# Performance work log

Hardware: AMD Instinct MI355X
Metric: run time of the kernel (lower is better)

The kernel has to match this reference:

```python
import jax, jax.numpy as jnp
import numpy as np

EMBED_DIM = 1024
NUM_HEADS = 16
D_K = EMBED_DIM // NUM_HEADS
FFN_DIM = 4096
EPS = 1e-5


def _linear_params(key, fan_in, fan_out):
    kw, kb = jax.random.split(key)
    bound = 1.0 / np.sqrt(fan_in)
    W = jax.random.uniform(kw, (fan_out, fan_in), jnp.float32, -bound, bound)
    b = jax.random.uniform(kb, (fan_out,), jnp.float32, -bound, bound)
    return W, b


def setup_inputs() -> dict:
    key = jax.random.key(0)
    ks = jax.random.split(key, 8)
    x = jax.random.normal(ks[0], (2, 2048, EMBED_DIM), jnp.float32)
    Wq, bq = _linear_params(ks[1], EMBED_DIM, EMBED_DIM)
    Wk, bk = _linear_params(ks[2], EMBED_DIM, EMBED_DIM)
    Wv, bv = _linear_params(ks[3], EMBED_DIM, EMBED_DIM)
    Wo, bo = _linear_params(ks[4], EMBED_DIM, EMBED_DIM)
    W1, b1 = _linear_params(ks[5], EMBED_DIM, FFN_DIM)
    W2, b2 = _linear_params(ks[6], FFN_DIM, EMBED_DIM)
    g1 = jnp.ones((EMBED_DIM,), jnp.float32)
    be1 = jnp.zeros((EMBED_DIM,), jnp.float32)
    g2 = jnp.ones((EMBED_DIM,), jnp.float32)
    be2 = jnp.zeros((EMBED_DIM,), jnp.float32)
    return {"x": x, "Wq": Wq, "bq": bq, "Wk": Wk, "bk": bk, "Wv": Wv, "bv": bv,
            "Wo": Wo, "bo": bo, "W1": W1, "b1": b1, "W2": W2, "b2": b2,
            "g1": g1, "be1": be1, "g2": g2, "be2": be2}


def _layernorm(x, g, b):
    mu = jnp.mean(x, axis=-1, keepdims=True)
    var = jnp.var(x, axis=-1, keepdims=True)
    return (x - mu) * jax.lax.rsqrt(var + EPS) * g + b


def reference(x, Wq, bq, Wk, bk, Wv, bv, Wo, bo, W1, b1, W2, b2, g1, be1, g2, be2):
    B, S, _ = x.shape
    h = _layernorm(x, g1, be1)
    # qkv projections -> [B, H, S, d_k]
    def split_heads(t):
        return t.reshape(B, S, NUM_HEADS, D_K).transpose(0, 2, 1, 3)
    q = split_heads(h @ Wq.T + bq)
    k = split_heads(h @ Wk.T + bk)
    v = split_heads(h @ Wv.T + bv)
    scores = jnp.einsum('bhqd,bhkd->bhqk', q, k) / np.sqrt(D_K).astype(np.float32)
    attn = jax.nn.softmax(scores, axis=-1)
    out = jnp.einsum('bhqk,bhkd->bhqd', attn, v)
    out = out.transpose(0, 2, 1, 3).reshape(B, S, EMBED_DIM)
    attn_out = out @ Wo.T + bo
    x = x + attn_out
    h2 = _layernorm(x, g2, be2)
    ffn = jax.nn.relu(h2 @ W1.T + b1) @ W2.T + b2
    return x + ffn
```

## Files before the change

kernel.cpp:

```cpp
#include <hip/hip_runtime.h>

typedef __attribute__((ext_vector_type(8))) short short8;
typedef __attribute__((ext_vector_type(4))) float f32x4;
typedef __attribute__((ext_vector_type(4))) unsigned short us4;

#define MFMA_BF16(a, b, c) __builtin_amdgcn_mfma_f32_16x16x32_bf16((a), (b), (c), 0, 0, 0)

__device__ __forceinline__ unsigned short f2bf(float f) {
  union { float f; unsigned int u; } x; x.f = f;
  unsigned int r = x.u + 0x7FFFu + ((x.u >> 16) & 1u);
  return (unsigned short)(r >> 16);
}
__device__ __forceinline__ float bf2f(unsigned short b) {
  union { float f; unsigned int u; } x; x.u = ((unsigned int)b) << 16;
  return x.f;
}

typedef __attribute__((address_space(3))) unsigned int lds_uint;
typedef const __attribute__((address_space(1))) unsigned int gbl_uint;

__device__ __forceinline__ void gload_lds16(const void* g, void* l) {
  __builtin_amdgcn_global_load_lds((gbl_uint*)g, (lds_uint*)l, 16, 0, 0);
}

__device__ __forceinline__ short8 lds_swz_read(const unsigned short* base, int row, int colbyte) {
  return *(const short8*)((const char*)base + row * 128 + (colbyte ^ ((row & 7) << 4)));
}

__global__ __launch_bounds__(256) void cvt_all(const float* __restrict__ Wq,
                                               const float* __restrict__ Wk,
                                               const float* __restrict__ Wv,
                                               const float* __restrict__ Wo,
                                               const float* __restrict__ W1,
                                               const float* __restrict__ W2,
                                               unsigned short* __restrict__ Wqkv_b,
                                               unsigned short* __restrict__ Wo_b,
                                               unsigned short* __restrict__ W1_b,
                                               unsigned short* __restrict__ W2_b) {
  const int b = blockIdx.x;
  const float* src;
  unsigned short* dst;
  int off;
  if (b < 1024)      { src = Wq; dst = Wqkv_b;           off = b; }
  else if (b < 2048) { src = Wk; dst = Wqkv_b + 1048576; off = b - 1024; }
  else if (b < 3072) { src = Wv; dst = Wqkv_b + 2097152; off = b - 2048; }
  else if (b < 4096) { src = Wo; dst = Wo_b;             off = b - 3072; }
  else if (b < 8192) { src = W1; dst = W1_b;             off = b - 4096; }
  else               { src = W2; dst = W2_b;             off = b - 8192; }
  const int i = off * 256 + threadIdx.x;
  const float4 v = ((const float4*)src)[i];
  us4 o;
  o.x = f2bf(v.x); o.y = f2bf(v.y); o.z = f2bf(v.z); o.w = f2bf(v.w);
  ((us4*)dst)[i] = o;
}

__global__ __launch_bounds__(256) void ln_kernel(const float* __restrict__ x,
                                                 const float* __restrict__ g,
                                                 const float* __restrict__ be,
                                                 unsigned short* __restrict__ out) {
  const int row = blockIdx.x;
  const int t = threadIdx.x;
  const float4 v = ((const float4*)(x + (size_t)row * 1024))[t];
  float s = v.x + v.y + v.z + v.w;
  float s2 = v.x * v.x + v.y * v.y + v.z * v.z + v.w * v.w;
#pragma unroll
  for (int d = 1; d < 64; d <<= 1) {
    s += __shfl_xor(s, d);
    s2 += __shfl_xor(s2, d);
  }
  __shared__ float red[8];
  const int wid = t >> 6, lane = t & 63;
  if (lane == 0) { red[wid] = s; red[4 + wid] = s2; }
  __syncthreads();
  s = red[0] + red[1] + red[2] + red[3];
  s2 = red[4] + red[5] + red[6] + red[7];
  const float mu = s * (1.0f / 1024.0f);
  const float var = s2 * (1.0f / 1024.0f) - mu * mu;
  const float rstd = rsqrtf(var + 1e-5f);
  const float4 gv = ((const float4*)g)[t];
  const float4 bv = ((const float4*)be)[t];
  us4 o;
  o.x = f2bf((v.x - mu) * rstd * gv.x + bv.x);
  o.y = f2bf((v.y - mu) * rstd * gv.y + bv.y);
  o.z = f2bf((v.z - mu) * rstd * gv.z + bv.z);
  o.w = f2bf((v.w - mu) * rstd * gv.w + bv.w);
  ((us4*)(out + (size_t)row * 1024))[t] = o;
}

__global__ __launch_bounds__(256) void ffn2_reduce(float* __restrict__ out,
                                                   const float* __restrict__ p1,
                                                   const float* __restrict__ x1,
                                                   const float* __restrict__ b2) {
  const int row = blockIdx.x, t = threadIdx.x;
  const size_t i = (size_t)row * 256 + t;
  float4 v = ((const float4*)out)[i];
  const float4 a = ((const float4*)p1)[i];
  const float4 c = ((const float4*)x1)[i];
  const float4 b = ((const float4*)b2)[t];
  v.x += a.x + c.x + b.x; v.y += a.y + c.y + b.y;
  v.z += a.z + c.z + b.z; v.w += a.w + c.w + b.w;
  ((float4*)out)[i] = v;
}

template <int BN, int EPI>
__global__ __launch_bounds__(256, 2) void gemm_bf16(const unsigned short* __restrict__ A,
                                                    const unsigned short* __restrict__ B,
                                                    const float* __restrict__ bias,
                                                    const float* __restrict__ biasK,
                                                    const float* __restrict__ biasV,
                                                    const float* __restrict__ res,
                                                    void* __restrict__ outp,
                                                    int M, int N, int K,
                                                    int gx, int gy, int kspl) {
  constexpr int WN = (BN == 128) ? 2 : 1;
  constexpr int WROWS = 128 / (4 / WN);
  constexpr int MW = WROWS / 16;
  constexpr int NW = (BN / WN) / 16;
  constexpr int BCH = BN / 32;
  constexpr int LOADS = 4 + BCH;

  __shared__ __align__(16) unsigned short As[2][128 * 64];
  __shared__ __align__(16) unsigned short Bs[2][BN * 64];

  const int nwg = gridDim.x;
  const int id2 = ((int)blockIdx.x & 7) * (nwg >> 3) + ((int)blockIdx.x >> 3);
  const int bx = id2 % gx;
  const int byz = id2 / gx;
  const int by = byz % gy;
  const int bz = byz / gy;

  const int wid = threadIdx.x >> 6;
  const int lane = threadIdx.x & 63;
  const int lr = lane & 15, lg = lane >> 4;
  const int row0 = by * 128;
  const int col0 = bx * BN;
  const int k0 = bz * kspl;
  const int wm = (wid / WN) * WROWS;
  const int wn = (wid % WN) * (BN / WN);

  const int scol = ((lane & 7) ^ ((lane >> 3) & 7)) * 8;

  auto stage = [&](int buf, int kt) {
#pragma unroll
    for (int i = 0; i < 4; ++i) {
      const int r = wid * 32 + i * 8;
      gload_lds16(A + (size_t)(row0 + r + (lane >> 3)) * K + kt + scol,
                  (void*)&As[buf][r * 64]);
    }
#pragma unroll
    for (int i = 0; i < BCH; ++i) {
      const int r = wid * (8 * BCH) + i * 8;
      gload_lds16(B + (size_t)(col0 + r + (lane >> 3)) * K + kt + scol,
                  (void*)&Bs[buf][r * 64]);
    }
  };

  f32x4 acc[MW][NW];
#pragma unroll
  for (int m = 0; m < MW; ++m)
#pragma unroll
    for (int n = 0; n < NW; ++n) acc[m][n] = (f32x4){0.f, 0.f, 0.f, 0.f};

  auto mma = [&](int buf) {
#pragma unroll
    for (int kk = 0; kk < 64; kk += 32) {
      const int colbyte = kk * 2 + lg * 16;
      short8 av[MW], bv[NW];
#pragma unroll
      for (int m = 0; m < MW; ++m)
        av[m] = lds_swz_read(&As[buf][0], wm + m * 16 + lr, colbyte);
#pragma unroll
      for (int n = 0; n < NW; ++n)
        bv[n] = lds_swz_read(&Bs[buf][0], wn + n * 16 + lr, colbyte);
#pragma unroll
      for (int m = 0; m < MW; ++m)
#pragma unroll
        for (int n = 0; n < NW; ++n) acc[m][n] = MFMA_BF16(av[m], bv[n], acc[m][n]);
    }
  };

  stage(0, k0);
  stage(1, k0 + 64);
  const int ktend = k0 + kspl;
  int cur = 0;
  for (int kt = k0; kt < ktend - 64; kt += 64) {
    asm volatile("s_waitcnt vmcnt(%0)" ::"i"(LOADS) : "memory");
    __builtin_amdgcn_s_barrier();
    __builtin_amdgcn_sched_barrier(0);
    mma(cur);
    __builtin_amdgcn_s_barrier();
    if (kt + 128 < ktend) stage(cur, kt + 128);
    cur ^= 1;
  }
  asm volatile("s_waitcnt vmcnt(0)" ::: "memory");
  __builtin_amdgcn_s_barrier();
  __builtin_amdgcn_sched_barrier(0);
  mma(cur);

#pragma unroll
  for (int m = 0; m < MW; ++m) {
#pragma unroll
    for (int n = 0; n < NW; ++n) {
#pragma unroll
      for (int r = 0; r < 4; ++r) {
        const int row = row0 + wm + m * 16 + lg * 4 + r;
        const int col = col0 + wn + n * 16 + lr;
        if constexpr (EPI == 0) {
          const int which = col >> 10, c = col & 1023;
          const float* bp = (which == 0) ? bias : (which == 1) ? biasK : biasV;
          const float v = acc[m][n][r] + bp[c];
          const size_t idx = (size_t)which * 4194304 +
              ((((size_t)(row >> 11)) * 16 + (c >> 6)) * 2048 + (row & 2047)) * 64 + (c & 63);
          ((unsigned short*)outp)[idx] = f2bf(v);
        } else if constexpr (EPI == 1) {
          const float v = acc[m][n][r] + bias[col];
          ((unsigned short*)outp)[(size_t)row * N + col] = f2bf(fmaxf(v, 0.f));
        } else {
          const float v = acc[m][n][r] + bias[col];
          ((float*)outp)[(size_t)row * N + col] = v + res[(size_t)row * N + col];
        }
      }
    }
  }
}

template <int BM, int BN, int EPI>
__global__ __launch_bounds__(512, 2) void gemm256(const unsigned short* __restrict__ A,
                                                  const unsigned short* __restrict__ B,
                                                  const float* __restrict__ bias,
                                                  float* __restrict__ part,
                                                  void* __restrict__ outp,
                                                  int M, int N, int K,
                                                  int gx, int gy, int kspl) {
  constexpr int MW = BM / 32;
  constexpr int NW = BN / 64;
  constexpr int A_ISS = BM / 64;
  constexpr int B_ISS = BN / 64;
  constexpr int LOADS = A_ISS + B_ISS;

  __shared__ __align__(16) unsigned short As[2][BM * 64];
  __shared__ __align__(16) unsigned short Bs[2][BN * 64];

  const int nwg = gridDim.x;
  const int id2 = ((int)blockIdx.x & 7) * (nwg >> 3) + ((int)blockIdx.x >> 3);
  const int bx = id2 % gx;
  const int byz = id2 / gx;
  const int by = byz % gy;
  const int bz = byz / gy;

  const int wid = threadIdx.x >> 6;
  const int lane = threadIdx.x & 63;
  const int lr = lane & 15, lg = lane >> 4;
  const int wr = wid >> 2, wc = wid & 3;
  const int row0 = by * BM;
  const int col0 = bx * BN;
  const int k0 = bz * kspl;
  const int wm = wr * (BM / 2);
  const int wn = wc * (BN / 4);

  const int scol = ((lane & 7) ^ ((lane >> 3) & 7)) * 8;

  auto stage = [&](int buf, int kt) {
#pragma unroll
    for (int i = 0; i < A_ISS; ++i) {
      const int r = wid * 8 + i * 64;
      gload_lds16(A + (size_t)(row0 + r + (lane >> 3)) * K + kt + scol,
                  (void*)&As[buf][r * 64]);
    }
#pragma unroll
    for (int i = 0; i < B_ISS; ++i) {
      const int r = wid * 8 + i * 64;
      gload_lds16(B + (size_t)(col0 + r + (lane >> 3)) * K + kt + scol,
                  (void*)&Bs[buf][r * 64]);
    }
  };

  f32x4 acc[MW][NW];
#pragma unroll
  for (int m = 0; m < MW; ++m)
#pragma unroll
    for (int n = 0; n < NW; ++n) acc[m][n] = (f32x4){0.f, 0.f, 0.f, 0.f};

  auto mma = [&](int buf) {
#pragma unroll
    for (int kk = 0; kk < 64; kk += 32) {
      const int colbyte = kk * 2 + lg * 16;
      short8 av[MW], bv[NW];
#pragma unroll
      for (int m = 0; m < MW; ++m)
        av[m] = lds_swz_read(&As[buf][0], wm + m * 16 + lr, colbyte);
#pragma unroll
      for (int n = 0; n < NW; ++n)
        bv[n] = lds_swz_read(&Bs[buf][0], wn + n * 16 + lr, colbyte);
#pragma unroll
      for (int m = 0; m < MW; ++m)
#pragma unroll
        for (int n = 0; n < NW; ++n) acc[m][n] = MFMA_BF16(av[m], bv[n], acc[m][n]);
    }
  };

  stage(0, k0);
  stage(1, k0 + 64);
  const int ktend = k0 + kspl;
  int cur = 0;
  for (int kt = k0; kt < ktend - 64; kt += 64) {
    asm volatile("s_waitcnt vmcnt(%0)" ::"i"(LOADS) : "memory");
    __builtin_amdgcn_s_barrier();
    __builtin_amdgcn_sched_barrier(0);
    mma(cur);
    __builtin_amdgcn_s_barrier();
    if (kt + 128 < ktend) stage(cur, kt + 128);
    cur ^= 1;
  }
  asm volatile("s_waitcnt vmcnt(0)" ::: "memory");
  __builtin_amdgcn_s_barrier();
  __builtin_amdgcn_sched_barrier(0);
  mma(cur);

#pragma unroll
  for (int m = 0; m < MW; ++m) {
#pragma unroll
    for (int n = 0; n < NW; ++n) {
#pragma unroll
      for (int r = 0; r < 4; ++r) {
        const int row = row0 + wm + m * 16 + lg * 4 + r;
        const int col = col0 + wn + n * 16 + lr;
        if constexpr (EPI == 1) {
          const float v = acc[m][n][r] + bias[col];
          ((unsigned short*)outp)[(size_t)row * N + col] = f2bf(fmaxf(v, 0.f));
        } else {
          float* dst = bz ? part : (float*)outp;
          dst[(size_t)row * N + col] = acc[m][n][r];
        }
      }
    }
  }
}

__global__ __launch_bounds__(256, 2) void attn_kernel(const unsigned short* __restrict__ q,
                                                      const unsigned short* __restrict__ k,
                                                      const unsigned short* __restrict__ v,
                                                      unsigned short* __restrict__ o) {
  const int bh = blockIdx.x;
  const int q0 = blockIdx.y * 128;
  const unsigned short* qh = q + (size_t)bh * 2048 * 64;
  const unsigned short* kh = k + (size_t)bh * 2048 * 64;
  const unsigned short* vh = v + (size_t)bh * 2048 * 64;
  const int wid = threadIdx.x >> 6, lane = threadIdx.x & 63;
  const int lr = lane & 15, lg = lane >> 4;
  const int qw = q0 + wid * 32;

  __shared__ __align__(16) unsigned short Vt[2][64 * 64];
  __shared__ __align__(16) unsigned short Ps[4][32 * 64];

  constexpr float CS = 0.125f * 1.4426950408889634f;
  short8 qf[2][2];
#pragma unroll
  for (int m = 0; m < 2; ++m)
#pragma unroll
    for (int kk = 0; kk < 2; ++kk) {
      short8 t = *(const short8*)&qh[(size_t)(qw + m * 16 + lr) * 64 + kk * 32 + lg * 8];
#pragma unroll
      for (int j = 0; j < 8; ++j) t[j] = (short)f2bf(bf2f((unsigned short)t[j]) * CS);
      qf[m][kk] = t;
    }

  f32x4 po[2][4];
  float lrun[2][4];
#pragma unroll
  for (int m = 0; m < 2; ++m) {
#pragma unroll
    for (int n = 0; n < 4; ++n) po[m][n] = (f32x4){0.f, 0.f, 0.f, 0.f};
#pragma unroll
    for (int r = 0; r < 4; ++r) lrun[m][r] = 0.f;
  }

  const int vd0 = wid * 16;
  const unsigned short* const vsrc = vh + (size_t)lane * 64 + vd0;
  const int sig2 = ((lane & 15) << 3) | ((lane >> 4) << 1);
  char* const PsB = (char*)&Ps[wid][0];

  short8 kfA[4][2], kfB[4][2], vA0, vA1, vB0, vB1;

#define LOAD_K(KF, kt)                                                                   \
  {                                                                                      \
    _Pragma("unroll") for (int n = 0; n < 4; ++n) _Pragma("unroll") for (int kk = 0;     \
                                                                         kk < 2; ++kk)  \
        KF[n][kk] =                                                                      \
        *(const short8*)&kh[(size_t)((kt) + n * 16 + lr) * 64 + kk * 32 + lg * 8];       \
  }
#define LOAD_V(V0, V1, kt)                                                               \
  {                                                                                      \
    V0 = *(const short8*)(vsrc + (size_t)(kt) * 64);                                     \
    V1 = *(const short8*)(vsrc + (size_t)(kt) * 64 + 8);                                 \
  }

  LOAD_K(kfA, 0)
  LOAD_V(vA0, vA1, 0)

#define STEP(KC, KN, VC0, VC1, VN0, VN1, BUF, t)                                         \
  {                                                                                      \
    char* const VtB = (char*)&Vt[BUF][0];                                                \
    _Pragma("unroll") for (int j = 0; j < 8; ++j) {                                      \
      const int row = vd0 + j;                                                           \
      *(unsigned short*)(VtB + row * 128 + (sig2 ^ ((row & 7) << 4))) =                  \
          (unsigned short)VC0[j];                                                        \
      const int row2 = vd0 + 8 + j;                                                      \
      *(unsigned short*)(VtB + row2 * 128 + (sig2 ^ ((row2 & 7) << 4))) =                \
          (unsigned short)VC1[j];                                                        \
    }                                                                                    \
    f32x4 sc[2][4];                                                                      \
    _Pragma("unroll") for (int m = 0; m < 2; ++m) _Pragma("unroll") for (int n = 0;      \
                                                                         n < 4; ++n)    \
        sc[m][n] = (f32x4){0.f, 0.f, 0.f, 0.f};                                          \
    __builtin_amdgcn_s_setprio(1);                                                       \
    _Pragma("unroll") for (int kk = 0; kk < 2; ++kk)                                     \
        _Pragma("unroll") for (int m = 0; m < 2; ++m)                                    \
        _Pragma("unroll") for (int n = 0; n < 4; ++n)                                    \
        sc[m][n] = MFMA_BF16(qf[m][kk], KC[n][kk], sc[m][n]);                            \
    __builtin_amdgcn_s_setprio(0);                                                       \
    const int ktn = ((t) + 1 < 32) ? ((t) + 1) * 64 : 0;                                 \
    LOAD_V(VN0, VN1, ktn)                                                                \
    LOAD_K(KN, ktn)                                                                      \
    _Pragma("unroll") for (int m = 0; m < 2; ++m)                                        \
        _Pragma("unroll") for (int r = 0; r < 4; ++r) {                                  \
      const float p0 = __builtin_amdgcn_exp2f(sc[m][0][r]);                              \
      const float p1 = __builtin_amdgcn_exp2f(sc[m][1][r]);                              \
      const float p2 = __builtin_amdgcn_exp2f(sc[m][2][r]);                              \
      const float p3 = __builtin_amdgcn_exp2f(sc[m][3][r]);                              \
      lrun[m][r] += (p0 + p1) + (p2 + p3);                                               \
      us4 pk;                                                                            \
      pk.x = f2bf(p0); pk.y = f2bf(p1); pk.z = f2bf(p2); pk.w = f2bf(p3);                \
      const int row = m * 16 + lg * 4 + r;                                               \
      *(us4*)(PsB + row * 128 + ((lr * 8) ^ ((row & 7) << 4))) = pk;                     \
    }                                                                                    \
    asm volatile("s_waitcnt lgkmcnt(0)" ::: "memory");                                   \
    __builtin_amdgcn_s_barrier();                                                        \
    __builtin_amdgcn_sched_barrier(0);                                                   \
    _Pragma("unroll") for (int kk = 0; kk < 2; ++kk) {                                   \
      const int coff = kk * 64 + lg * 16;                                                \
      short8 pa[2], vbr[4];                                                              \
      _Pragma("unroll") for (int m = 0; m < 2; ++m) {                                    \
        const int prow = m * 16 + lr;                                                    \
        pa[m] = *(const short8*)(PsB + prow * 128 + (coff ^ ((prow & 7) << 4)));         \
      }                                                                                  \
      _Pragma("unroll") for (int n = 0; n < 4; ++n) {                                    \
        const int vrow = n * 16 + lr;                                                    \
        vbr[n] = *(const short8*)(VtB + vrow * 128 + (coff ^ ((vrow & 7) << 4)));        \
      }                                                                                  \
      __builtin_amdgcn_s_setprio(1);                                                     \
      _Pragma("unroll") for (int m = 0; m < 2; ++m)                                      \
          _Pragma("unroll") for (int n = 0; n < 4; ++n)                                  \
          po[m][n] = MFMA_BF16(pa[m], vbr[n], po[m][n]);                                 \
      __builtin_amdgcn_s_setprio(0);                                                     \
    }                                                                                    \
  }

  for (int t = 0; t < 32; t += 2) {
    STEP(kfA, kfB, vA0, vA1, vB0, vB1, 0, t)
    STEP(kfB, kfA, vB0, vB1, vA0, vA1, 1, t + 1)
  }
#undef STEP
#undef LOAD_K
#undef LOAD_V

#pragma unroll
  for (int d = 1; d < 16; d <<= 1)
#pragma unroll
    for (int m = 0; m < 2; ++m)
#pragma unroll
      for (int r = 0; r < 4; ++r) lrun[m][r] += __shfl_xor(lrun[m][r], d);

  const int b = bh >> 4, hh = bh & 15;
#pragma unroll
  for (int m = 0; m < 2; ++m)
#pragma unroll
    for (int n = 0; n < 4; ++n)
#pragma unroll
      for (int r = 0; r < 4; ++r) {
        const int qrow = qw + m * 16 + lg * 4 + r;
        const int d = n * 16 + lr;
        o[((size_t)b * 2048 + qrow) * 1024 + hh * 64 + d] =
            f2bf(po[m][n][r] / lrun[m][r]);
      }
}

extern "C" void kernel_launch(void* const* d_in, const int* in_sizes, int n_in,
                              void* d_out, int out_size, void* d_ws, size_t ws_size,
                              hipStream_t stream) {
  const float* x  = (const float*)d_in[0];
  const float* Wq = (const float*)d_in[1];
  const float* bq = (const float*)d_in[2];
  const float* Wk = (const float*)d_in[3];
  const float* bk = (const float*)d_in[4];
  const float* Wv = (const float*)d_in[5];
  const float* bv = (const float*)d_in[6];
  const float* Wo = (const float*)d_in[7];
  const float* bo = (const float*)d_in[8];
  const float* W1 = (const float*)d_in[9];
  const float* b1 = (const float*)d_in[10];
  const float* W2 = (const float*)d_in[11];
  const float* b2 = (const float*)d_in[12];
  const float* g1 = (const float*)d_in[13];
  const float* be1 = (const float*)d_in[14];
  const float* g2 = (const float*)d_in[15];
  const float* be2 = (const float*)d_in[16];

  char* ws = (char*)d_ws;
  const size_t MB = 1024 * 1024;
  unsigned short* Wqkv_b = (unsigned short*)(ws + 0 * MB);
  unsigned short* Wo_b   = (unsigned short*)(ws + 6 * MB);
  unsigned short* W1_b   = (unsigned short*)(ws + 8 * MB);
  unsigned short* W2_b   = (unsigned short*)(ws + 16 * MB);
  unsigned short* h_b    = (unsigned short*)(ws + 24 * MB);
  unsigned short* qb     = (unsigned short*)(ws + 32 * MB);
  unsigned short* ab     = (unsigned short*)(ws + 56 * MB);
  float*          x1     = (float*)(ws + 64 * MB);
  unsigned short* fb     = (unsigned short*)(ws + 32 * MB);
  float*          p1     = (float*)(ws + 0 * MB);

  cvt_all<<<12288, 256, 0, stream>>>(Wq, Wk, Wv, Wo, W1, W2, Wqkv_b, Wo_b, W1_b, W2_b);

  ln_kernel<<<4096, 256, 0, stream>>>(x, g1, be1, h_b);

  gemm_bf16<128, 0><<<768, 256, 0, stream>>>(h_b, Wqkv_b, bq, bk, bv, nullptr, qb,
                                             4096, 3072, 1024, 24, 32, 1024);

  attn_kernel<<<dim3(32, 16), 256, 0, stream>>>(qb, qb + 4194304, qb + 2 * 4194304, ab);

  gemm_bf16<64, 2><<<512, 256, 0, stream>>>(ab, Wo_b, bo, nullptr, nullptr, x, x1,
                                            4096, 1024, 1024, 16, 32, 1024);

  ln_kernel<<<4096, 256, 0, stream>>>(x1, g2, be2, h_b);

  gemm256<256, 256, 1><<<256, 512, 0, stream>>>(h_b, W1_b, b1, nullptr, fb,
                                                4096, 4096, 1024, 16, 16, 1024);

  gemm256<128, 256, 4><<<256, 512, 0, stream>>>(fb, W2_b, nullptr, p1, (float*)d_out,
                                                4096, 1024, 4096, 4, 32, 2048);

  ffn2_reduce<<<4096, 256, 0, stream>>>((float*)d_out, p1, x1, b2);
}
```

Baseline: 249.8 us.

## Split attention over two KV slices and add a combine kernel

Each attention block now covers half of the key/value sequence, which doubles the grid from 512 to 1024 blocks. Each block writes unnormalized bf16 partial outputs and fp32 row sums to workspace. A new combine kernel adds the two partials, divides by the summed normalizer and writes the head-interleaved output. The goal is better CU occupancy for attention. The costs are an extra launch, extra global traffic for the partials, and rounding of the partials to bf16 before normalization. The combine is only correct if both slices use the same softmax offset.

```diff
diff --git a/kernel.cpp b/kernel.cpp
--- a/kernel.cpp
+++ b/kernel.cpp
@@ -102,6 +102,26 @@
   ((float4*)out)[i] = v;
 }
 
+__global__ __launch_bounds__(256) void attn_combine(const unsigned short* __restrict__ opart,
+                                                    const float* __restrict__ lpart,
+                                                    unsigned short* __restrict__ o) {
+  const int bh = blockIdx.x;
+  const int row = blockIdx.y * 16 + (threadIdx.x >> 4);
+  const int d0 = (threadIdx.x & 15) * 4;
+  const size_t i0 = (size_t)bh * 2048 + row;
+  const size_t i1 = (size_t)(32 + bh) * 2048 + row;
+  const us4 a = *(const us4*)&opart[i0 * 64 + d0];
+  const us4 b = *(const us4*)&opart[i1 * 64 + d0];
+  const float linv = 1.0f / (lpart[i0] + lpart[i1]);
+  const int bb = bh >> 4, hh = bh & 15;
+  us4 r;
+  r.x = f2bf((bf2f(a.x) + bf2f(b.x)) * linv);
+  r.y = f2bf((bf2f(a.y) + bf2f(b.y)) * linv);
+  r.z = f2bf((bf2f(a.z) + bf2f(b.z)) * linv);
+  r.w = f2bf((bf2f(a.w) + bf2f(b.w)) * linv);
+  *(us4*)&o[((size_t)bb * 2048 + row) * 1024 + hh * 64 + d0] = r;
+}
+
 template <int BN, int EPI>
 __global__ __launch_bounds__(256, 2) void gemm_bf16(const unsigned short* __restrict__ A,
                                                     const unsigned short* __restrict__ B,
@@ -340,9 +360,14 @@
 __global__ __launch_bounds__(256, 2) void attn_kernel(const unsigned short* __restrict__ q,
                                                       const unsigned short* __restrict__ k,
                                                       const unsigned short* __restrict__ v,
-                                                      unsigned short* __restrict__ o) {
+                                                      unsigned short* __restrict__ opart,
+                                                      float* __restrict__ lpart) {
   const int bh = blockIdx.x;
-  const int q0 = blockIdx.y * 128;
+  const int yb = blockIdx.y;
+  const int q0 = (yb & 15) * 128;
+  const int slice = yb >> 4;
+  const int s0 = slice * 16;
+  const int send = s0 + 16;
   const unsigned short* qh = q + (size_t)bh * 2048 * 64;
   const unsigned short* kh = k + (size_t)bh * 2048 * 64;
   const unsigned short* vh = v + (size_t)bh * 2048 * 64;
@@ -395,8 +420,8 @@
     V1 = *(const short8*)(vsrc + (size_t)(kt) * 64 + 8);                                 \
   }
 
-  LOAD_K(kfA, 0)
-  LOAD_V(vA0, vA1, 0)
+  LOAD_K(kfA, s0 * 64)
+  LOAD_V(vA0, vA1, s0 * 64)
 
 #define STEP(KC, KN, VC0, VC1, VN0, VN1, BUF, t)                                         \
   {                                                                                      \
@@ -419,7 +444,7 @@
         _Pragma("unroll") for (int n = 0; n < 4; ++n)                                    \
         sc[m][n] = MFMA_BF16(qf[m][kk], KC[n][kk], sc[m][n]);                            \
     __builtin_amdgcn_s_setprio(0);                                                       \
-    const int ktn = ((t) + 1 < 32) ? ((t) + 1) * 64 : 0;                                 \
+    const int ktn = ((t) + 1 < send) ? ((t) + 1) * 64 : s0 * 64;                         \
     LOAD_V(VN0, VN1, ktn)                                                                \
     LOAD_K(KN, ktn)                                                                      \
     _Pragma("unroll") for (int m = 0; m < 2; ++m)                                        \
@@ -456,7 +481,7 @@
     }                                                                                    \
   }
 
-  for (int t = 0; t < 32; t += 2) {
+  for (int t = s0; t < send; t += 2) {
     STEP(kfA, kfB, vA0, vA1, vB0, vB1, 0, t)
     STEP(kfB, kfA, vB0, vB1, vA0, vA1, 1, t + 1)
   }
@@ -471,7 +496,7 @@
 #pragma unroll
       for (int r = 0; r < 4; ++r) lrun[m][r] += __shfl_xor(lrun[m][r], d);
 
-  const int b = bh >> 4, hh = bh & 15;
+  const size_t obase = ((size_t)slice * 32 + bh) * 2048;
 #pragma unroll
   for (int m = 0; m < 2; ++m)
 #pragma unroll
@@ -479,10 +504,15 @@
 #pragma unroll
       for (int r = 0; r < 4; ++r) {
         const int qrow = qw + m * 16 + lg * 4 + r;
-        const int d = n * 16 + lr;
-        o[((size_t)b * 2048 + qrow) * 1024 + hh * 64 + d] =
-            f2bf(po[m][n][r] / lrun[m][r]);
+        opart[(obase + qrow) * 64 + n * 16 + lr] = f2bf(po[m][n][r]);
       }
+  if (lr == 0) {
+#pragma unroll
+    for (int m = 0; m < 2; ++m)
+#pragma unroll
+      for (int r = 0; r < 4; ++r)
+        lpart[obase + qw + m * 16 + lg * 4 + r] = lrun[m][r];
+  }
 }
 
 extern "C" void kernel_launch(void* const* d_in, const int* in_sizes, int n_in,
@@ -518,6 +548,8 @@
   float*          x1     = (float*)(ws + 64 * MB);
   unsigned short* fb     = (unsigned short*)(ws + 32 * MB);
   float*          p1     = (float*)(ws + 0 * MB);
+  unsigned short* opart  = (unsigned short*)(ws + 64 * MB);
+  float*          lpart  = (float*)(ws + 0 * MB);
 
   cvt_all<<<12288, 256, 0, stream>>>(Wq, Wk, Wv, Wo, W1, W2, Wqkv_b, Wo_b, W1_b, W2_b);
 
@@ -526,7 +558,10 @@
   gemm_bf16<128, 0><<<768, 256, 0, stream>>>(h_b, Wqkv_b, bq, bk, bv, nullptr, qb,
                                              4096, 3072, 1024, 24, 32, 1024);
 
-  attn_kernel<<<dim3(32, 16), 256, 0, stream>>>(qb, qb + 4194304, qb + 2 * 4194304, ab);
+  attn_kernel<<<dim3(32, 32), 256, 0, stream>>>(qb, qb + 4194304, qb + 2 * 4194304,
+                                                opart, lpart);
+
+  attn_combine<<<dim3(32, 128), 256, 0, stream>>>(opart, lpart, ab);
 
   gemm_bf16<64, 2><<<512, 256, 0, stream>>>(ab, Wo_b, bo, nullptr, nullptr, x, x1,
                                             4096, 1024, 1024, 16, 32, 1024);
```

After: 259.1 us. +3.7%, slower.
